# Kernel optimization log

Measured on AMD Instinct MI355X. Metric: run time of the kernel, lower is better.

## Reference

```python
import jax, jax.numpy as jnp
import numpy as np

B, T, D, H = 4, 2048, 1024, 16
HD = D // H  # head_size = 64


def setup_inputs() -> dict:
    key = jax.random.key(0)
    ks = jax.random.split(key, 6)
    s = 0.02
    x = jax.random.normal(ks[0], (B, T, D), dtype=jnp.float32)
    # per-head unfused projections, stacked over heads: [H, D, HD]
    Wq = jax.random.normal(ks[1], (H, D, HD), dtype=jnp.float32) * s
    Wk = jax.random.normal(ks[2], (H, D, HD), dtype=jnp.float32) * s
    Wv = jax.random.normal(ks[3], (H, D, HD), dtype=jnp.float32) * s
    # output projection, torch Linear layout [out, in]
    Wo = jax.random.normal(ks[4], (D, D), dtype=jnp.float32) * s
    bo = jax.random.normal(ks[5], (D,), dtype=jnp.float32) * s
    return {"x": x, "Wq": Wq, "Wk": Wk, "Wv": Wv, "Wo": Wo, "bo": bo}


def reference(x, Wq, Wk, Wv, Wo, bo):
    b, t, d = x.shape
    hd = Wq.shape[-1]
    q = jnp.einsum('btd,hdk->bhtk', x, Wq)
    k = jnp.einsum('btd,hdk->bhtk', x, Wk)
    v = jnp.einsum('btd,hdk->bhtk', x, Wv)
    scores = jnp.einsum('bhtk,bhsk->bhts', q, k) / jnp.sqrt(jnp.float32(hd))
    mask = jnp.tril(jnp.ones((t, t), dtype=bool))  # causal
    scores = jnp.where(mask, scores, jnp.float32(-jnp.inf))
    p = jax.nn.softmax(scores, axis=-1)
    o = jnp.einsum('bhts,bhsk->bhtk', p, v)
    o = o.transpose(0, 2, 1, 3).reshape(b, t, d)  # concat heads
    return o @ Wo.T + bo
```

## Files before the change

kernel.cpp:

```cpp
#include <hip/hip_runtime.h>
#include <hip/hip_bf16.h>
#include <stdint.h>

#define B_   4
#define T_   2048
#define D_   1024
#define H_   16
#define HD_  64
#define MROWS (B_*T_)
#define NQKV  3072
#define NST  (T_/64)

typedef __attribute__((ext_vector_type(8))) short  short8;
typedef __attribute__((ext_vector_type(4))) short  bf16x4;
typedef __attribute__((ext_vector_type(4))) float  floatx4;

#define QSCALE 0.1803368801111244f

__device__ inline void async_copy16(const __hip_bfloat16* g, __hip_bfloat16* l) {
  __builtin_amdgcn_global_load_lds(
      (const __attribute__((address_space(1))) void*)g,
      (__attribute__((address_space(3))) void*)l, 16, 0, 0);
}

__device__ inline floatx4 mfma16(bf16x4 a, bf16x4 b, floatx4 c) {
#if __has_builtin(__builtin_amdgcn_mfma_f32_16x16x16bf16_1k)
  return __builtin_amdgcn_mfma_f32_16x16x16bf16_1k(a, b, c, 0, 0, 0);
#elif __has_builtin(__builtin_amdgcn_mfma_f32_16x16x16_bf16)
  return __builtin_amdgcn_mfma_f32_16x16x16_bf16(a, b, c, 0, 0, 0);
#else
  short8 a8 = (short8){a[0], a[1], a[2], a[3], 0, 0, 0, 0};
  short8 b8 = (short8){b[0], b[1], b[2], b[3], 0, 0, 0, 0};
  return __builtin_amdgcn_mfma_f32_16x16x32_bf16(a8, b8, c, 0, 0, 0);
#endif
}


__global__ void convert_bf16(const float* __restrict__ in, __hip_bfloat16* __restrict__ out, int n) {
  int i = (blockIdx.x * blockDim.x + threadIdx.x) * 4;
  if (i < n) {
    float4 v = *(const float4*)(in + i);
    out[i + 0] = __float2bfloat16(v.x);
    out[i + 1] = __float2bfloat16(v.y);
    out[i + 2] = __float2bfloat16(v.z);
    out[i + 3] = __float2bfloat16(v.w);
  }
}

__global__ void transpose_w(const float* __restrict__ Wq, const float* __restrict__ Wk,
                            const float* __restrict__ Wv, __hip_bfloat16* __restrict__ wqkv) {
  __shared__ __hip_bfloat16 tile[64][65];
  const int t = threadIdx.x;
  const int d0 = blockIdx.x * 64;
  const int wh = blockIdx.y;
  const int which = wh >> 4, h = wh & 15;
  const float* W = (which == 0) ? Wq : ((which == 1) ? Wk : Wv);
  const float* base = W + (size_t)h * D_ * HD_;
#pragma unroll
  for (int i = 0; i < 16; i++) {
    int e = i * 256 + t;
    int dr = e >> 6, hd = e & 63;
    tile[dr][hd] = __float2bfloat16(base[(size_t)(d0 + dr) * HD_ + hd]);
  }
  __syncthreads();
#pragma unroll
  for (int i = 0; i < 16; i++) {
    int e = i * 256 + t;
    int hd = e >> 6, dr = e & 63;
    wqkv[(size_t)(which * 1024 + h * 64 + hd) * D_ + d0 + dr] = tile[dr][hd];
  }
}

__global__ void repack_kv(const __hip_bfloat16* __restrict__ qkv,
                          __hip_bfloat16* __restrict__ kpack, __hip_bfloat16* __restrict__ vpack) {
  __shared__ __hip_bfloat16 Ks[64][72];
  __shared__ __hip_bfloat16 Vs[64][72];
  const int tid = threadIdx.x;
  const int st = blockIdx.x, bh = blockIdx.y;
  const int b = bh >> 4, h = bh & 15;
#pragma unroll
  for (int p = 0; p < 2; p++) {
    int c = p * 256 + tid;
    int row = c >> 3, col8 = c & 7;
    const __hip_bfloat16* src = qkv + (size_t)(b * T_ + st * 64 + row) * NQKV + h * HD_ + col8 * 8;
    *(uint4*)&Ks[row][col8 * 8] = *(const uint4*)(src + 1024);
    *(uint4*)&Vs[row][col8 * 8] = *(const uint4*)(src + 2048);
  }
  __syncthreads();
  const size_t base = ((size_t)bh * NST + st) * 8 * 512;
#pragma unroll
  for (int p = 0; p < 2; p++) {
    int pair = p * 256 + tid;
    int c = pair >> 6, l = pair & 63;
    int lq = l & 15, q = l >> 4;
    int ni = c >> 1, half = c & 1;
    short8 v = *(const short8*)&Ks[ni * 16 + lq][half * 32 + q * 8];
    *(short8*)(kpack + base + (size_t)c * 512 + l * 8) = v;
  }
#pragma unroll
  for (int p = 0; p < 2; p++) {
    int pair = p * 256 + tid;
    int c = pair >> 6, l = pair & 63;
    int lq = l & 15, q = l >> 4;
    int m = c >> 2, nt = c & 3;
    __hip_bfloat16 tmp[8];
#pragma unroll
    for (int half = 0; half < 2; half++)
#pragma unroll
      for (int j = 0; j < 4; j++)
        tmp[half * 4 + j] = Vs[(2 * m + half) * 16 + q * 4 + j][nt * 16 + lq];
    *(short8*)(vpack + base + (size_t)c * 512 + l * 8) = *(short8*)tmp;
  }
}

template <int EPI>
__launch_bounds__(256, 2)
__global__ void gemm_bt(const __hip_bfloat16* __restrict__ A, const __hip_bfloat16* __restrict__ Bt,
                        __hip_bfloat16* __restrict__ Cb, float* __restrict__ Cf,
                        const float* __restrict__ bias, int M, int N, int K, float qscale) {
  __shared__ __hip_bfloat16 As[128 * 32];
  __shared__ __hip_bfloat16 Bs[128 * 32];
  const int tid = threadIdx.x;
  const int w = tid >> 6, lane = tid & 63;
  const int lq = lane & 15, quad = lane >> 4;
  const int wr = w >> 1, wc = w & 1;
  const int m0 = blockIdx.x * 128, n0 = blockIdx.y * 128;

  floatx4 acc[4][4];
#pragma unroll
  for (int i = 0; i < 4; i++)
#pragma unroll
    for (int j = 0; j < 4; j++) acc[i][j] = (floatx4){0.f, 0.f, 0.f, 0.f};

  for (int k0 = 0; k0 < K; k0 += 32) {
    __syncthreads();
#pragma unroll
    for (int ph = 0; ph < 2; ++ph) {
      int c = ph * 256 + tid;
      int row = c >> 2, col8 = c & 3;
      async_copy16(A + (size_t)(m0 + row) * K + k0 + col8 * 8, As + c * 8);
      async_copy16(Bt + (size_t)(n0 + row) * K + k0 + col8 * 8, Bs + c * 8);
    }
    __syncthreads();
    short8 af[4], bf[4];
#pragma unroll
    for (int mi = 0; mi < 4; mi++)
      af[mi] = *(const short8*)(As + (wr * 64 + mi * 16 + lq) * 32 + quad * 8);
#pragma unroll
    for (int ni = 0; ni < 4; ni++)
      bf[ni] = *(const short8*)(Bs + (wc * 64 + ni * 16 + lq) * 32 + quad * 8);
#pragma unroll
    for (int mi = 0; mi < 4; mi++)
#pragma unroll
      for (int ni = 0; ni < 4; ni++)
        acc[mi][ni] = __builtin_amdgcn_mfma_f32_16x16x32_bf16(af[mi], bf[ni], acc[mi][ni], 0, 0, 0);
  }

#pragma unroll
  for (int mi = 0; mi < 4; mi++) {
#pragma unroll
    for (int ni = 0; ni < 4; ni++) {
      int col = n0 + wc * 64 + ni * 16 + lq;
      if (EPI == 0) {
        float s = (col < 1024) ? qscale : 1.0f;
#pragma unroll
        for (int r = 0; r < 4; r++) {
          int row = m0 + wr * 64 + mi * 16 + quad * 4 + r;
          Cb[(size_t)row * N + col] = __float2bfloat16(acc[mi][ni][r] * s);
        }
      } else {
        float bv = bias[col];
#pragma unroll
        for (int r = 0; r < 4; r++) {
          int row = m0 + wr * 64 + mi * 16 + quad * 4 + r;
          Cf[(size_t)row * N + col] = acc[mi][ni][r] + bv;
        }
      }
    }
  }
}

__launch_bounds__(256, 2)
__global__ void attn(const __hip_bfloat16* __restrict__ qkv,
                     const __hip_bfloat16* __restrict__ kpack,
                     const __hip_bfloat16* __restrict__ vpack,
                     __hip_bfloat16* __restrict__ obuf) {
  const int tid = threadIdx.x;
  const int w = tid >> 6, lane = tid & 63;
  const int lq = lane & 15, quad = lane >> 4;

  const int bh = (int)blockIdx.x;
  const int a  = (int)blockIdx.y;
  const int b = bh >> 4, h = bh & 15;

  const __hip_bfloat16* kb0 = kpack + ((size_t)bh * NST) * 4096 + lane * 8;
  const __hip_bfloat16* vb0 = vpack + ((size_t)bh * NST) * 4096 + lane * 8;

#pragma unroll 1
  for (int seg = 0; seg < 2; ++seg) {
    const int tbase = seg ? (NST - 2 - 2 * a) : (2 * a);
    const int qt = tbase + (w >> 1);
    const int rbase = (w & 1) * 32;

    short8 qf[2][2];
#pragma unroll
    for (int bi = 0; bi < 2; bi++) {
      const __hip_bfloat16* qp =
          qkv + ((size_t)(b * T_ + qt * 64 + rbase + bi * 16 + lq)) * NQKV + h * HD_;
      qf[bi][0] = *(const short8*)(qp + quad * 8);
      qf[bi][1] = *(const short8*)(qp + 32 + quad * 8);
    }

    floatx4 Oacc[2][4];
#pragma unroll
    for (int bi = 0; bi < 2; bi++)
#pragma unroll
      for (int i = 0; i < 4; i++) Oacc[bi][i] = (floatx4){0.f, 0.f, 0.f, 0.f};
    float lrow[2] = {0.f, 0.f};

    const __hip_bfloat16* kb = kb0;
    const __hip_bfloat16* vb = vb0;
    const int nIter = qt + 1;
    for (int it = 0; it < nIter; ++it) {
      short8 kf[4], kg[4];
#pragma unroll
      for (int ni = 0; ni < 4; ni++) {
        kf[ni] = *(const short8*)(kb + (size_t)(ni * 2 + 0) * 512);
        kg[ni] = *(const short8*)(kb + (size_t)(ni * 2 + 1) * 512);
      }
      short8 vfr[8];
#pragma unroll
      for (int c = 0; c < 8; c++) vfr[c] = *(const short8*)(vb + (size_t)c * 512);

      floatx4 Sc[2][4];
#pragma unroll
      for (int bi = 0; bi < 2; bi++)
#pragma unroll
        for (int ni = 0; ni < 4; ni++) {
          floatx4 c0 = (floatx4){0.f, 0.f, 0.f, 0.f};
          c0 = __builtin_amdgcn_mfma_f32_16x16x32_bf16(kf[ni], qf[bi][0], c0, 0, 0, 0);
          c0 = __builtin_amdgcn_mfma_f32_16x16x32_bf16(kg[ni], qf[bi][1], c0, 0, 0, 0);
          Sc[bi][ni] = c0;
        }

      if (it == nIter - 1) {
#pragma unroll
        for (int bi = 0; bi < 2; bi++) {
          int lrow_idx = rbase + bi * 16 + lq;
#pragma unroll
          for (int ni = 0; ni < 4; ni++)
#pragma unroll
            for (int r = 0; r < 4; r++) {
              int s_loc = ni * 16 + quad * 4 + r;
              if (s_loc > lrow_idx) Sc[bi][ni][r] = -__builtin_inff();
            }
        }
      }

      bf16x4 pf[2][4];
#pragma unroll
      for (int bi = 0; bi < 2; bi++)
#pragma unroll
        for (int c = 0; c < 4; c++) {
          __hip_bfloat16 pb[4];
#pragma unroll
          for (int r = 0; r < 4; r++) {
            float p = __builtin_amdgcn_exp2f(Sc[bi][c][r]);
            lrow[bi] += p;
            pb[r] = __float2bfloat16(p);
          }
          pf[bi][c] = *(bf16x4*)pb;
        }

#pragma unroll
      for (int m = 0; m < 2; m++)
#pragma unroll
        for (int nt = 0; nt < 4; nt++) {
          short8 v8 = vfr[m * 4 + nt];
          bf16x4 vlo = (bf16x4){v8[0], v8[1], v8[2], v8[3]};
          bf16x4 vhi = (bf16x4){v8[4], v8[5], v8[6], v8[7]};
#pragma unroll
          for (int bi = 0; bi < 2; bi++) {
            Oacc[bi][nt] = mfma16(pf[bi][2 * m + 0], vlo, Oacc[bi][nt]);
            Oacc[bi][nt] = mfma16(pf[bi][2 * m + 1], vhi, Oacc[bi][nt]);
          }
        }

      kb += 4096;
      vb += 4096;
    }

#pragma unroll
    for (int bi = 0; bi < 2; bi++) {
      float ps = lrow[bi];
      ps += __shfl_xor(ps, 16);
      ps += __shfl_xor(ps, 32);
      float inv = 1.0f / ps;
#pragma unroll
      for (int r = 0; r < 4; r++) {
        float invr = __shfl(inv, quad * 4 + r);
        int t = qt * 64 + rbase + bi * 16 + quad * 4 + r;
#pragma unroll
        for (int nt = 0; nt < 4; nt++)
          obuf[(size_t)(b * T_ + t) * D_ + h * HD_ + nt * 16 + lq] =
              __float2bfloat16(Oacc[bi][nt][r] * invr);
      }
    }
  }
}


extern "C" void kernel_launch(void* const* d_in, const int* in_sizes, int n_in,
                              void* d_out, int out_size, void* d_ws, size_t ws_size,
                              hipStream_t stream) {
  const float* x  = (const float*)d_in[0];
  const float* Wq = (const float*)d_in[1];
  const float* Wk = (const float*)d_in[2];
  const float* Wv = (const float*)d_in[3];
  const float* Wo = (const float*)d_in[4];
  const float* bo = (const float*)d_in[5];
  float* out = (float*)d_out;

  char* ws = (char*)d_ws;
  __hip_bfloat16* xb    = (__hip_bfloat16*)(ws);
  __hip_bfloat16* obuf  = (__hip_bfloat16*)(ws);
  __hip_bfloat16* wqkv  = (__hip_bfloat16*)(ws + ((size_t)16 << 20));
  __hip_bfloat16* wob   = (__hip_bfloat16*)(ws + ((size_t)22 << 20));
  __hip_bfloat16* qkv   = (__hip_bfloat16*)(ws + ((size_t)24 << 20));
  __hip_bfloat16* kpack = (__hip_bfloat16*)(ws + ((size_t)72 << 20));
  __hip_bfloat16* vpack = (__hip_bfloat16*)(ws + ((size_t)88 << 20));

  convert_bf16<<<(MROWS * D_) / 1024, 256, 0, stream>>>(x, xb, MROWS * D_);
  convert_bf16<<<(D_ * D_) / 1024, 256, 0, stream>>>(Wo, wob, D_ * D_);
  transpose_w<<<dim3(16, 48), 256, 0, stream>>>(Wq, Wk, Wv, wqkv);

  gemm_bt<0><<<dim3(MROWS / 128, NQKV / 128), 256, 0, stream>>>(
      xb, wqkv, qkv, nullptr, nullptr, MROWS, NQKV, D_, QSCALE);

  repack_kv<<<dim3(NST, B_ * H_), 256, 0, stream>>>(qkv, kpack, vpack);

  attn<<<dim3(B_ * H_, 8), 256, 0, stream>>>(qkv, kpack, vpack, obuf);

  gemm_bt<1><<<dim3(MROWS / 128, D_ / 128), 256, 0, stream>>>(
      obuf, wob, nullptr, out, bo, MROWS, D_, D_, 1.0f);
}
```

Baseline: 249.7 us.

## Split attention KV range across wave pairs and deepen GEMM K tile

Measured after the change: 305.4 us. 1.22x slower.

```diff
diff --git a/kernel.cpp b/kernel.cpp
--- a/kernel.cpp
+++ b/kernel.cpp
@@ -118,8 +118,8 @@
 __global__ void gemm_bt(const __hip_bfloat16* __restrict__ A, const __hip_bfloat16* __restrict__ Bt,
                         __hip_bfloat16* __restrict__ Cb, float* __restrict__ Cf,
                         const float* __restrict__ bias, int M, int N, int K, float qscale) {
-  __shared__ __hip_bfloat16 As[128 * 32];
-  __shared__ __hip_bfloat16 Bs[128 * 32];
+  __shared__ __hip_bfloat16 As[128 * 64];
+  __shared__ __hip_bfloat16 Bs[128 * 64];
   const int tid = threadIdx.x;
   const int w = tid >> 6, lane = tid & 63;
   const int lq = lane & 15, quad = lane >> 4;
@@ -132,28 +132,31 @@
 #pragma unroll
     for (int j = 0; j < 4; j++) acc[i][j] = (floatx4){0.f, 0.f, 0.f, 0.f};
 
-  for (int k0 = 0; k0 < K; k0 += 32) {
+  for (int k0 = 0; k0 < K; k0 += 64) {
     __syncthreads();
 #pragma unroll
-    for (int ph = 0; ph < 2; ++ph) {
+    for (int ph = 0; ph < 4; ++ph) {
       int c = ph * 256 + tid;
-      int row = c >> 2, col8 = c & 3;
+      int row = c >> 3, col8 = c & 7;
       async_copy16(A + (size_t)(m0 + row) * K + k0 + col8 * 8, As + c * 8);
       async_copy16(Bt + (size_t)(n0 + row) * K + k0 + col8 * 8, Bs + c * 8);
     }
     __syncthreads();
-    short8 af[4], bf[4];
-#pragma unroll
-    for (int mi = 0; mi < 4; mi++)
-      af[mi] = *(const short8*)(As + (wr * 64 + mi * 16 + lq) * 32 + quad * 8);
-#pragma unroll
-    for (int ni = 0; ni < 4; ni++)
-      bf[ni] = *(const short8*)(Bs + (wc * 64 + ni * 16 + lq) * 32 + quad * 8);
-#pragma unroll
-    for (int mi = 0; mi < 4; mi++)
+#pragma unroll
+    for (int kh = 0; kh < 2; kh++) {
+      short8 af[4], bf[4];
+#pragma unroll
+      for (int mi = 0; mi < 4; mi++)
+        af[mi] = *(const short8*)(As + (wr * 64 + mi * 16 + lq) * 64 + kh * 32 + quad * 8);
 #pragma unroll
       for (int ni = 0; ni < 4; ni++)
-        acc[mi][ni] = __builtin_amdgcn_mfma_f32_16x16x32_bf16(af[mi], bf[ni], acc[mi][ni], 0, 0, 0);
+        bf[ni] = *(const short8*)(Bs + (wc * 64 + ni * 16 + lq) * 64 + kh * 32 + quad * 8);
+#pragma unroll
+      for (int mi = 0; mi < 4; mi++)
+#pragma unroll
+        for (int ni = 0; ni < 4; ni++)
+          acc[mi][ni] = __builtin_amdgcn_mfma_f32_16x16x32_bf16(af[mi], bf[ni], acc[mi][ni], 0, 0, 0);
+    }
   }
 
 #pragma unroll
@@ -180,14 +183,17 @@
   }
 }
 
-__launch_bounds__(256, 2)
+__launch_bounds__(256, 4)
 __global__ void attn(const __hip_bfloat16* __restrict__ qkv,
                      const __hip_bfloat16* __restrict__ kpack,
                      const __hip_bfloat16* __restrict__ vpack,
                      __hip_bfloat16* __restrict__ obuf) {
+  __shared__ float Osh[2][64][34];
+
   const int tid = threadIdx.x;
   const int w = tid >> 6, lane = tid & 63;
   const int lq = lane & 15, quad = lane >> 4;
+  const int rh = w & 1, sh = w >> 1;
 
   const int bh = (int)blockIdx.x;
   const int a  = (int)blockIdx.y;
@@ -198,9 +204,13 @@
 
 #pragma unroll 1
   for (int seg = 0; seg < 2; ++seg) {
-    const int tbase = seg ? (NST - 2 - 2 * a) : (2 * a);
-    const int qt = tbase + (w >> 1);
-    const int rbase = (w & 1) * 32;
+    const int qt = seg ? (NST - 1 - a) : a;
+    const int rbase = rh * 32;
+
+    const int nIter = qt + 1;
+    const int half = (nIter + 1) >> 1;
+    const int it0 = sh ? half : 0;
+    const int it1 = sh ? nIter : half;
 
     short8 qf[2][2];
 #pragma unroll
@@ -218,10 +228,10 @@
       for (int i = 0; i < 4; i++) Oacc[bi][i] = (floatx4){0.f, 0.f, 0.f, 0.f};
     float lrow[2] = {0.f, 0.f};
 
-    const __hip_bfloat16* kb = kb0;
-    const __hip_bfloat16* vb = vb0;
-    const int nIter = qt + 1;
-    for (int it = 0; it < nIter; ++it) {
+    const __hip_bfloat16* kb = kb0 + (size_t)it0 * 4096;
+    const __hip_bfloat16* vb = vb0 + (size_t)it0 * 4096;
+
+    for (int it = it0; it < it1; ++it) {
       short8 kf[4], kg[4];
 #pragma unroll
       for (int ni = 0; ni < 4; ni++) {
@@ -290,22 +300,46 @@
       vb += 4096;
     }
 
-#pragma unroll
-    for (int bi = 0; bi < 2; bi++) {
-      float ps = lrow[bi];
-      ps += __shfl_xor(ps, 16);
-      ps += __shfl_xor(ps, 32);
-      float inv = 1.0f / ps;
-#pragma unroll
-      for (int r = 0; r < 4; r++) {
-        float invr = __shfl(inv, quad * 4 + r);
-        int t = qt * 64 + rbase + bi * 16 + quad * 4 + r;
+    if (sh == 1) {
+#pragma unroll
+      for (int bi = 0; bi < 2; bi++)
 #pragma unroll
         for (int nt = 0; nt < 4; nt++)
-          obuf[(size_t)(b * T_ + t) * D_ + h * HD_ + nt * 16 + lq] =
-              __float2bfloat16(Oacc[bi][nt][r] * invr);
-      }
-    }
+#pragma unroll
+          for (int r = 0; r < 4; r++)
+            Osh[rh][lane][bi * 16 + nt * 4 + r] = Oacc[bi][nt][r];
+      Osh[rh][lane][32] = lrow[0];
+      Osh[rh][lane][33] = lrow[1];
+    }
+    __syncthreads();
+    if (sh == 0) {
+#pragma unroll
+      for (int bi = 0; bi < 2; bi++) {
+#pragma unroll
+        for (int nt = 0; nt < 4; nt++)
+#pragma unroll
+          for (int r = 0; r < 4; r++)
+            Oacc[bi][nt][r] += Osh[rh][lane][bi * 16 + nt * 4 + r];
+        lrow[bi] += Osh[rh][lane][32 + bi];
+      }
+#pragma unroll
+      for (int bi = 0; bi < 2; bi++) {
+        float ps = lrow[bi];
+        ps += __shfl_xor(ps, 16);
+        ps += __shfl_xor(ps, 32);
+        float inv = 1.0f / ps;
+#pragma unroll
+        for (int r = 0; r < 4; r++) {
+          float invr = __shfl(inv, quad * 4 + r);
+          int t = qt * 64 + rbase + bi * 16 + quad * 4 + r;
+#pragma unroll
+          for (int nt = 0; nt < 4; nt++)
+            obuf[(size_t)(b * T_ + t) * D_ + h * HD_ + nt * 16 + lq] =
+                __float2bfloat16(Oacc[bi][nt][r] * invr);
+        }
+      }
+    }
+    __syncthreads();
   }
 }
 
@@ -339,7 +373,7 @@
 
   repack_kv<<<dim3(NST, B_ * H_), 256, 0, stream>>>(qkv, kpack, vpack);
 
-  attn<<<dim3(B_ * H_, 8), 256, 0, stream>>>(qkv, kpack, vpack, obuf);
+  attn<<<dim3(B_ * H_, 16), 256, 0, stream>>>(qkv, kpack, vpack, obuf);
 
   gemm_bt<1><<<dim3(MROWS / 128, D_ / 128), 256, 0, stream>>>(
       obuf, wob, nullptr, out, bo, MROWS, D_, D_, 1.0f);
```

## Double-buffer K/V register loads in attention and widen GEMM K-tile to 64

Applied to the files above, without the earlier changes.

Result: slower. 264.9 us (+6.1%).

```diff
diff --git a/kernel.cpp b/kernel.cpp
--- a/kernel.cpp
+++ b/kernel.cpp
@@ -118,8 +118,8 @@
 __global__ void gemm_bt(const __hip_bfloat16* __restrict__ A, const __hip_bfloat16* __restrict__ Bt,
                         __hip_bfloat16* __restrict__ Cb, float* __restrict__ Cf,
                         const float* __restrict__ bias, int M, int N, int K, float qscale) {
-  __shared__ __hip_bfloat16 As[128 * 32];
-  __shared__ __hip_bfloat16 Bs[128 * 32];
+  __shared__ __hip_bfloat16 As[128 * 64];
+  __shared__ __hip_bfloat16 Bs[128 * 64];
   const int tid = threadIdx.x;
   const int w = tid >> 6, lane = tid & 63;
   const int lq = lane & 15, quad = lane >> 4;
@@ -132,28 +132,31 @@
 #pragma unroll
     for (int j = 0; j < 4; j++) acc[i][j] = (floatx4){0.f, 0.f, 0.f, 0.f};
 
-  for (int k0 = 0; k0 < K; k0 += 32) {
+  for (int k0 = 0; k0 < K; k0 += 64) {
     __syncthreads();
 #pragma unroll
-    for (int ph = 0; ph < 2; ++ph) {
+    for (int ph = 0; ph < 4; ++ph) {
       int c = ph * 256 + tid;
-      int row = c >> 2, col8 = c & 3;
+      int row = c >> 3, col8 = c & 7;
       async_copy16(A + (size_t)(m0 + row) * K + k0 + col8 * 8, As + c * 8);
       async_copy16(Bt + (size_t)(n0 + row) * K + k0 + col8 * 8, Bs + c * 8);
     }
     __syncthreads();
-    short8 af[4], bf[4];
-#pragma unroll
-    for (int mi = 0; mi < 4; mi++)
-      af[mi] = *(const short8*)(As + (wr * 64 + mi * 16 + lq) * 32 + quad * 8);
-#pragma unroll
-    for (int ni = 0; ni < 4; ni++)
-      bf[ni] = *(const short8*)(Bs + (wc * 64 + ni * 16 + lq) * 32 + quad * 8);
-#pragma unroll
-    for (int mi = 0; mi < 4; mi++)
+#pragma unroll
+    for (int kh = 0; kh < 2; kh++) {
+      short8 af[4], bf[4];
+#pragma unroll
+      for (int mi = 0; mi < 4; mi++)
+        af[mi] = *(const short8*)(As + (wr * 64 + mi * 16 + lq) * 64 + kh * 32 + quad * 8);
 #pragma unroll
       for (int ni = 0; ni < 4; ni++)
-        acc[mi][ni] = __builtin_amdgcn_mfma_f32_16x16x32_bf16(af[mi], bf[ni], acc[mi][ni], 0, 0, 0);
+        bf[ni] = *(const short8*)(Bs + (wc * 64 + ni * 16 + lq) * 64 + kh * 32 + quad * 8);
+#pragma unroll
+      for (int mi = 0; mi < 4; mi++)
+#pragma unroll
+        for (int ni = 0; ni < 4; ni++)
+          acc[mi][ni] = __builtin_amdgcn_mfma_f32_16x16x32_bf16(af[mi], bf[ni], acc[mi][ni], 0, 0, 0);
+    }
   }
 
 #pragma unroll
@@ -221,17 +224,8 @@
     const __hip_bfloat16* kb = kb0;
     const __hip_bfloat16* vb = vb0;
     const int nIter = qt + 1;
-    for (int it = 0; it < nIter; ++it) {
-      short8 kf[4], kg[4];
-#pragma unroll
-      for (int ni = 0; ni < 4; ni++) {
-        kf[ni] = *(const short8*)(kb + (size_t)(ni * 2 + 0) * 512);
-        kg[ni] = *(const short8*)(kb + (size_t)(ni * 2 + 1) * 512);
-      }
-      short8 vfr[8];
-#pragma unroll
-      for (int c = 0; c < 8; c++) vfr[c] = *(const short8*)(vb + (size_t)c * 512);
-
+
+    auto body = [&](const short8* kf, const short8* kg, const short8* vfr, int it) {
       floatx4 Sc[2][4];
 #pragma unroll
       for (int bi = 0; bi < 2; bi++)
@@ -242,7 +236,6 @@
           c0 = __builtin_amdgcn_mfma_f32_16x16x32_bf16(kg[ni], qf[bi][1], c0, 0, 0, 0);
           Sc[bi][ni] = c0;
         }
-
       if (it == nIter - 1) {
 #pragma unroll
         for (int bi = 0; bi < 2; bi++) {
@@ -256,7 +249,6 @@
             }
         }
       }
-
       bf16x4 pf[2][4];
 #pragma unroll
       for (int bi = 0; bi < 2; bi++)
@@ -271,7 +263,6 @@
           }
           pf[bi][c] = *(bf16x4*)pb;
         }
-
 #pragma unroll
       for (int m = 0; m < 2; m++)
 #pragma unroll
@@ -285,9 +276,30 @@
             Oacc[bi][nt] = mfma16(pf[bi][2 * m + 1], vhi, Oacc[bi][nt]);
           }
         }
-
-      kb += 4096;
-      vb += 4096;
+    };
+
+    auto loadset = [&](short8* kf, short8* kg, short8* vfr, const __hip_bfloat16* kp,
+                       const __hip_bfloat16* vp) {
+#pragma unroll
+      for (int ni = 0; ni < 4; ni++) {
+        kf[ni] = *(const short8*)(kp + (size_t)(ni * 2 + 0) * 512);
+        kg[ni] = *(const short8*)(kp + (size_t)(ni * 2 + 1) * 512);
+      }
+#pragma unroll
+      for (int c = 0; c < 8; c++) vfr[c] = *(const short8*)(vp + (size_t)c * 512);
+    };
+
+    short8 kfA[4], kgA[4], vfA[8], kfB[4], kgB[4], vfB[8];
+    loadset(kfA, kgA, vfA, kb, vb);
+    int it = 0;
+    while (it < nIter) {
+      if (it + 1 < nIter) loadset(kfB, kgB, vfB, kb + 4096, vb + 4096);
+      body(kfA, kgA, vfA, it);
+      kb += 4096; vb += 4096; ++it;
+      if (it >= nIter) break;
+      if (it + 1 < nIter) loadset(kfA, kgA, vfA, kb + 4096, vb + 4096);
+      body(kfB, kgB, vfB, it);
+      kb += 4096; vb += 4096; ++it;
     }
 
 #pragma unroll
```
